# Kernel tuning notes

Hardware: AMD Instinct MI355X
Metric: run time of the kernel (lower is better)

The kernel has to match this reference:

```python
import jax, jax.numpy as jnp
import numpy as np

B, IN_F, OUT_F = 16384, 2048, 8192


def setup_inputs() -> dict:
    key = jax.random.key(0)
    kx, kw, kb = jax.random.split(key, 3)
    bound = 1.0 / np.sqrt(IN_F)
    x = jax.random.normal(kx, (B, IN_F), dtype=jnp.float32)
    # nn.Linear default init: U(-1/sqrt(in), 1/sqrt(in)); W is (out, in)
    W = jax.random.uniform(kw, (OUT_F, IN_F), dtype=jnp.float32, minval=-bound, maxval=bound)
    b = jax.random.uniform(kb, (OUT_F,), dtype=jnp.float32, minval=-bound, maxval=bound)
    return {"x": x, "W": W, "b": b}


def reference(x, W, b):
    # Linear: (B, in) @ (in, out) + (out,) -> (B, out)
    y = jnp.einsum("bi,oi->bo", x, W) + b
    # Fused full-row sum reduction -> (B, 1)
    return jnp.sum(y, axis=-1, keepdims=True)
```

## Files before the change

kernel.cpp:

```cpp
#include <hip/hip_runtime.h>


#define B_ROWS 16384
#define IN_F   2048
#define OUT_F  8192

constexpr int ROWS_PER_CHUNK = 32;
constexpr int N_CHUNKS   = OUT_F / ROWS_PER_CHUNK;
constexpr int F4_PER_ROW = IN_F / 4;

constexpr int WS_P = N_CHUNKS * IN_F;

__global__ __launch_bounds__(256) void colsum_partial(const float* __restrict__ W,
                                                      float* __restrict__ ws) {
    const int h     = blockIdx.x & 1;
    const int chunk = blockIdx.x >> 1;
    const int col4  = h * 256 + threadIdx.x;

    const float4* W4 = reinterpret_cast<const float4*>(W);
    long base = (long)chunk * ROWS_PER_CHUNK * F4_PER_ROW + col4;

    float4 acc = make_float4(0.f, 0.f, 0.f, 0.f);
#pragma unroll
    for (int r = 0; r < ROWS_PER_CHUNK; ++r) {
        float4 v = W4[base + (long)r * F4_PER_ROW];
        acc.x += v.x; acc.y += v.y; acc.z += v.z; acc.w += v.w;
    }
    reinterpret_cast<float4*>(ws)[(long)chunk * F4_PER_ROW + col4] = acc;
}

__global__ __launch_bounds__(256) void reduce_kernel(const float* __restrict__ b,
                                                     float* __restrict__ ws) {
    if (blockIdx.x == IN_F / 256) {
        __shared__ float red[4];
        float acc = 0.f;
        for (int i = threadIdx.x; i < OUT_F; i += 256) acc += b[i];
#pragma unroll
        for (int off = 32; off > 0; off >>= 1) acc += __shfl_down(acc, off);
        if ((threadIdx.x & 63) == 0) red[threadIdx.x >> 6] = acc;
        __syncthreads();
        if (threadIdx.x == 0) ws[WS_P + IN_F] = red[0] + red[1] + red[2] + red[3];
        return;
    }
    const int col = blockIdx.x * 256 + threadIdx.x;
    float acc = 0.f;
    for (int c = 0; c < N_CHUNKS; ++c) acc += ws[(long)c * IN_F + col];
    ws[WS_P + col] = acc;
}

__global__ __launch_bounds__(256) void gemv_kernel(const float* __restrict__ x,
                                                   const float* __restrict__ ws,
                                                   float* __restrict__ out) {
    const int wave = threadIdx.x >> 6;
    const int lane = threadIdx.x & 63;
    const int row  = blockIdx.x * 4 + wave;

    const float4* x4 = reinterpret_cast<const float4*>(x + (long)row * IN_F);
    const float4* c4 = reinterpret_cast<const float4*>(ws + WS_P);

    float acc = 0.f;
#pragma unroll
    for (int it = 0; it < IN_F / 4 / 64; ++it) {
        const int idx = it * 64 + lane;
        float4 xv = x4[idx];
        float4 cv = c4[idx];
        acc += xv.x * cv.x + xv.y * cv.y + xv.z * cv.z + xv.w * cv.w;
    }
#pragma unroll
    for (int off = 32; off > 0; off >>= 1) acc += __shfl_down(acc, off);
    if (lane == 0) out[row] = acc + ws[WS_P + IN_F];
}

extern "C" void kernel_launch(void* const* d_in, const int* in_sizes, int n_in,
                              void* d_out, int out_size, void* d_ws, size_t ws_size,
                              hipStream_t stream) {
    const float* x = (const float*)d_in[0];
    const float* W = (const float*)d_in[1];
    const float* b = (const float*)d_in[2];
    float* out = (float*)d_out;
    float* ws  = (float*)d_ws;

    colsum_partial<<<2 * N_CHUNKS, 256, 0, stream>>>(W, ws);
    reduce_kernel<<<IN_F / 256 + 1, 256, 0, stream>>>(b, ws);
    gemv_kernel<<<B_ROWS / 4, 256, 0, stream>>>(x, ws, out);
}
```

Baseline: 246.3 us.

## Split column-sum reduction across more blocks with atomic accumulation

Halves rows per chunk and has each colsum block process both halves of a row, doubling the partial-sum count. The second-stage reduction now spreads across 64 blocks that each sum a slice of chunks and atomically add into a zeroed buffer, replacing 9 blocks that serially summed all chunks. This removes a long serial dependent-load loop with little parallelism, at the cost of a memset, a larger partial workspace and float atomics that make summation order nondeterministic.

```diff
diff --git a/kernel.cpp b/kernel.cpp
--- a/kernel.cpp
+++ b/kernel.cpp
@@ -5,33 +5,38 @@
 #define IN_F   2048
 #define OUT_F  8192
 
-constexpr int ROWS_PER_CHUNK = 32;
+constexpr int ROWS_PER_CHUNK = 16;
 constexpr int N_CHUNKS   = OUT_F / ROWS_PER_CHUNK;
 constexpr int F4_PER_ROW = IN_F / 4;
 
-constexpr int WS_P = N_CHUNKS * IN_F;
+constexpr long WS_P = (long)N_CHUNKS * IN_F;
 
 __global__ __launch_bounds__(256) void colsum_partial(const float* __restrict__ W,
                                                       float* __restrict__ ws) {
-    const int h     = blockIdx.x & 1;
-    const int chunk = blockIdx.x >> 1;
-    const int col4  = h * 256 + threadIdx.x;
+    const int chunk = blockIdx.x;
+    const int t     = threadIdx.x;
 
     const float4* W4 = reinterpret_cast<const float4*>(W);
-    long base = (long)chunk * ROWS_PER_CHUNK * F4_PER_ROW + col4;
+    long base = (long)chunk * ROWS_PER_CHUNK * F4_PER_ROW;
 
-    float4 acc = make_float4(0.f, 0.f, 0.f, 0.f);
+    float4 a0 = make_float4(0.f, 0.f, 0.f, 0.f);
+    float4 a1 = make_float4(0.f, 0.f, 0.f, 0.f);
 #pragma unroll
     for (int r = 0; r < ROWS_PER_CHUNK; ++r) {
-        float4 v = W4[base + (long)r * F4_PER_ROW];
-        acc.x += v.x; acc.y += v.y; acc.z += v.z; acc.w += v.w;
+        float4 v0 = W4[base + (long)r * F4_PER_ROW + t];
+        float4 v1 = W4[base + (long)r * F4_PER_ROW + t + 256];
+        a0.x += v0.x; a0.y += v0.y; a0.z += v0.z; a0.w += v0.w;
+        a1.x += v1.x; a1.y += v1.y; a1.z += v1.z; a1.w += v1.w;
     }
-    reinterpret_cast<float4*>(ws)[(long)chunk * F4_PER_ROW + col4] = acc;
+    float4* P = reinterpret_cast<float4*>(ws);
+    P[(long)chunk * F4_PER_ROW + t]       = a0;
+    P[(long)chunk * F4_PER_ROW + t + 256] = a1;
 }
 
 __global__ __launch_bounds__(256) void reduce_kernel(const float* __restrict__ b,
                                                      float* __restrict__ ws) {
-    if (blockIdx.x == IN_F / 256) {
+    constexpr int CHUNKS_PER_BLK = N_CHUNKS / 8;
+    if (blockIdx.x == 64) {
         __shared__ float red[4];
         float acc = 0.f;
         for (int i = threadIdx.x; i < OUT_F; i += 256) acc += b[i];
@@ -42,10 +47,13 @@
         if (threadIdx.x == 0) ws[WS_P + IN_F] = red[0] + red[1] + red[2] + red[3];
         return;
     }
-    const int col = blockIdx.x * 256 + threadIdx.x;
+    const int col = (blockIdx.x & 7) * 256 + threadIdx.x;
+    const int c0  = (blockIdx.x >> 3) * CHUNKS_PER_BLK;
     float acc = 0.f;
-    for (int c = 0; c < N_CHUNKS; ++c) acc += ws[(long)c * IN_F + col];
-    ws[WS_P + col] = acc;
+#pragma unroll
+    for (int c = 0; c < CHUNKS_PER_BLK; ++c)
+        acc += ws[(long)(c0 + c) * IN_F + col];
+    atomicAdd(&ws[WS_P + col], acc);
 }
 
 __global__ __launch_bounds__(256) void gemv_kernel(const float* __restrict__ x,
@@ -80,7 +88,9 @@
     float* out = (float*)d_out;
     float* ws  = (float*)d_ws;
 
-    colsum_partial<<<2 * N_CHUNKS, 256, 0, stream>>>(W, ws);
-    reduce_kernel<<<IN_F / 256 + 1, 256, 0, stream>>>(b, ws);
+    hipMemsetAsync(ws + WS_P, 0, IN_F * sizeof(float), stream);
+
+    colsum_partial<<<N_CHUNKS, 256, 0, stream>>>(W, ws);
+    reduce_kernel<<<65, 256, 0, stream>>>(b, ws);
     gemv_kernel<<<B_ROWS / 4, 256, 0, stream>>>(x, ws, out);
 }
```

Result: no change. 250.4 us (+1.7%).
